# Optimization experiments

Hardware: AMD Instinct MI355X
Metric: run time of the kernel (lower is better)

The kernel has to match this reference:

```python
import jax, jax.numpy as jnp
import numpy as np

N, E, IN, HID, OUT, L = 50000, 800000, 128, 64, 40, 3


def setup_inputs() -> dict:
    key = jax.random.key(0)
    ks = jax.random.split(key, 10)
    x = jax.random.normal(ks[0], (N, IN), jnp.float32)
    edge_index = jax.random.randint(ks[1], (2, E), 0, N, dtype=jnp.int32)

    def u(k, shape, fan_in):
        s = 1.0 / np.sqrt(fan_in)
        return jax.random.uniform(k, shape, jnp.float32, -s, s)

    return {
        "x": x,
        "edge_index": edge_index,
        # former1 (NWGformerF): in -> hidden projection
        "Wf": u(ks[2], (IN, HID), IN),
        "bf": jnp.zeros((HID,), jnp.float32),
        # stacked GCNConv weights (hidden->hidden)
        "conv_W": u(ks[3], (L, HID, HID), HID),
        "conv_b": jnp.zeros((L, HID), jnp.float32),
        # residual linears
        "lin_W": u(ks[4], (L, HID, HID), HID),
        "lin_b": u(ks[5], (L, HID), HID),
        # batchnorm (eval mode: affine with running stats)
        "gamma": jnp.ones((L, HID), jnp.float32),
        "beta": jnp.zeros((L, HID), jnp.float32),
        "run_mean": jnp.zeros((L, HID), jnp.float32),
        "run_var": jnp.ones((L, HID), jnp.float32),
        # output head
        "pred_W": u(ks[6], (HID, OUT), HID),
        "pred_b": jnp.zeros((OUT,), jnp.float32),
    }


def reference(x, edge_index, Wf, bf, conv_W, conv_b, lin_W, lin_b,
              gamma, beta, run_mean, run_var, pred_W, pred_b):
    n = x.shape[0]
    src, dst = edge_index[0], edge_index[1]
    eps = 1e-5

    # GCN symmetric normalization with self-loops: deg over dst (+1 self loop)
    deg = jax.ops.segment_sum(jnp.ones(src.shape[0], x.dtype), dst,
                              num_segments=n) + 1.0
    dinv = jax.lax.rsqrt(deg)                      # [N]
    edge_coef = dinv[src] * dinv[dst]              # [E]
    self_coef = (dinv * dinv)[:, None]             # [N,1]

    def gcn(h, W, b):
        hw = h @ W                                 # [N,HID]
        agg = jax.ops.segment_sum(hw[src] * edge_coef[:, None], dst,
                                  num_segments=n)
        return agg + hw * self_coef + b

    # former1: in -> hidden (dropout is identity in eval mode)
    h = x @ Wf + bf

    for i in range(L):
        h = gcn(h, conv_W[i], conv_b[i]) + h @ lin_W[i] + lin_b[i]  # res
        h = (h - run_mean[i]) * (gamma[i] * jax.lax.rsqrt(run_var[i] + eps)) + beta[i]
        h = jax.nn.relu(h)

    return h @ pred_W + pred_b
```

## Files before the change

kernel.cpp:

```cpp
#include <hip/hip_runtime.h>
#include <hip/hip_bf16.h>
#include <hip/hip_fp16.h>

#define IN_DIM 128
#define HID 64
#define OUT_DIM 40
#define SPAD 68

typedef __hip_bfloat16 bf16;
typedef unsigned short u16;

__device__ __forceinline__ float b2f(bf16 v) { return __bfloat162float(v); }
__device__ __forceinline__ float relu_f(float x) { return 0.5f * (x + fabsf(x)); }
__device__ __forceinline__ float ldv(const void* p, int i, int is32) {
    return is32 ? ((const float*)p)[i] : b2f(((const bf16*)p)[i]);
}

__global__ void MPNNs_60198261620971_kernel() {}

__global__ void canary_k(float* out, int m) {
    int i = blockIdx.x * blockDim.x + threadIdx.x;
    if (i < m) out[i] = 1234.0f;
}

__global__ void detect_k(const unsigned int* __restrict__ rv, int* __restrict__ flag) {
    if (threadIdx.x == 0 && blockIdx.x == 0)
        flag[0] = (rv[0] == 0x3F800000u) ? 1 : 0;
}


__global__ void zero1_k(int* a, int n) {
    int i = blockIdx.x * blockDim.x + threadIdx.x;
    if (i < n) a[i] = 0;
}

__global__ void count_k(const int* __restrict__ dst, int* __restrict__ counts,
                        int* __restrict__ rank, int e, int n) {
    int i = blockIdx.x * blockDim.x + threadIdx.x;
    if (i < e) {
        int d = dst[i];
        int r = ((unsigned)d < (unsigned)n) ? atomicAdd(&counts[d], 1) : 0;
        rank[i] = r;
    }
}

__global__ void scan1_k(const int* __restrict__ counts, int* __restrict__ row_ptr,
                        int* __restrict__ psum, float* __restrict__ dinv, int n) {
    __shared__ int sdata[1024];
    int i = blockIdx.x * 1024 + threadIdx.x;
    int v = (i < n) ? counts[i] : 0;
    if (i < n) dinv[i] = rsqrtf((float)v + 1.0f);
    sdata[threadIdx.x] = v;
    __syncthreads();
    for (int off = 1; off < 1024; off <<= 1) {
        int t = (threadIdx.x >= off) ? sdata[threadIdx.x - off] : 0;
        __syncthreads();
        sdata[threadIdx.x] += t;
        __syncthreads();
    }
    if (i < n) row_ptr[i] = sdata[threadIdx.x] - v;
    if (threadIdx.x == 1023) psum[blockIdx.x] = sdata[1023];
}

__global__ void scan2_k(int* __restrict__ psum, int* __restrict__ row_ptr, int nb, int n) {
    __shared__ int sdata[1024];
    int v = (threadIdx.x < nb) ? psum[threadIdx.x] : 0;
    sdata[threadIdx.x] = v;
    __syncthreads();
    for (int off = 1; off < 1024; off <<= 1) {
        int t = (threadIdx.x >= off) ? sdata[threadIdx.x - off] : 0;
        __syncthreads();
        sdata[threadIdx.x] += t;
        __syncthreads();
    }
    if (threadIdx.x < nb) psum[threadIdx.x] = sdata[threadIdx.x] - v;
    if (threadIdx.x == 1023) row_ptr[n] = sdata[1023];
}

__global__ void scan3_k(int* __restrict__ row_ptr, const int* __restrict__ psum, int n) {
    int i = blockIdx.x * blockDim.x + threadIdx.x;
    if (i < n) row_ptr[i] += psum[i >> 10];
}

__global__ void fill_k(const int* __restrict__ src, const int* __restrict__ dst,
                       const int* __restrict__ row_ptr, const int* __restrict__ rank,
                       u16* __restrict__ col, int e, int n) {
    int i = blockIdx.x * blockDim.x + threadIdx.x;
    if (i < e) {
        int d = dst[i];
        if ((unsigned)d < (unsigned)n)
            col[row_ptr[d] + rank[i]] = (u16)src[i];
    }
}


__global__ __launch_bounds__(256) void former_k(const void* __restrict__ x,
                                                const void* __restrict__ Wf,
                                                const void* __restrict__ bfv,
                                                const int* __restrict__ dflag,
                                                float* __restrict__ h, int n) {
    __shared__ float sW[IN_DIM * HID];
    __shared__ float sx[64 * SPAD];
    int is32 = dflag[0];
    if (is32) {
        const float4* w4 = (const float4*)Wf;
        for (int i = threadIdx.x; i < IN_DIM * HID / 4; i += 256) ((float4*)sW)[i] = w4[i];
    } else {
        for (int i = threadIdx.x; i < IN_DIM * HID; i += 256) sW[i] = b2f(((const bf16*)Wf)[i]);
    }
    int tid = threadIdx.x, cg = tid & 15, rg = tid >> 4;
    int rowBase = blockIdx.x * 64;
    float acc[4][4];
    #pragma unroll
    for (int i = 0; i < 4; i++)
        #pragma unroll
        for (int j = 0; j < 4; j++) acc[i][j] = 0.f;

    for (int p = 0; p < 2; p++) {
        __syncthreads();
        #pragma unroll
        for (int pass = 0; pass < 4; pass++) {
            int r = pass * 16 + (tid >> 4);
            int c = (tid & 15) * 4;
            int gr = rowBase + r;
            float4 v = make_float4(0.f, 0.f, 0.f, 0.f);
            if (gr < n) {
                if (is32) v = *(const float4*)((const float*)x + (size_t)gr * IN_DIM + p * 64 + c);
                else {
                    const bf16* xb = (const bf16*)x + (size_t)gr * IN_DIM + p * 64 + c;
                    v = make_float4(b2f(xb[0]), b2f(xb[1]), b2f(xb[2]), b2f(xb[3]));
                }
            }
            *(float4*)&sx[r * SPAD + c] = v;
        }
        __syncthreads();
        for (int k = 0; k < 64; k += 4) {
            float4 hr[4], w[4];
            #pragma unroll
            for (int i = 0; i < 4; i++) hr[i] = *(float4*)&sx[(rg * 4 + i) * SPAD + k];
            #pragma unroll
            for (int j = 0; j < 4; j++) w[j] = *(float4*)&sW[(p * 64 + k + j) * HID + cg * 4];
            #pragma unroll
            for (int i = 0; i < 4; i++) {
                const float* hh = (const float*)&hr[i];
                #pragma unroll
                for (int j = 0; j < 4; j++) {
                    const float* ww = (const float*)&w[j];
                    acc[i][0] += hh[j] * ww[0];
                    acc[i][1] += hh[j] * ww[1];
                    acc[i][2] += hh[j] * ww[2];
                    acc[i][3] += hh[j] * ww[3];
                }
            }
        }
    }
    float b0 = ldv(bfv, cg * 4 + 0, is32), b1 = ldv(bfv, cg * 4 + 1, is32);
    float b2 = ldv(bfv, cg * 4 + 2, is32), b3 = ldv(bfv, cg * 4 + 3, is32);
    #pragma unroll
    for (int i = 0; i < 4; i++) {
        int r = rowBase + rg * 4 + i;
        if (r < n) {
            float4 o = make_float4(acc[i][0] + b0, acc[i][1] + b1, acc[i][2] + b2, acc[i][3] + b3);
            *(float4*)&h[(size_t)r * HID + cg * 4] = o;
        }
    }
}

__global__ __launch_bounds__(256) void dense_k(float* __restrict__ h,
                                               const void* __restrict__ convW,
                                               const void* __restrict__ linW,
                                               const void* __restrict__ convB,
                                               const void* __restrict__ linB,
                                               const int* __restrict__ dflag,
                                               const float* __restrict__ dinv,
                                               __half* __restrict__ hws, int n, int l) {
    __shared__ float sW1[HID * HID];
    __shared__ float sW2[HID * HID];
    __shared__ float sh[64 * SPAD];
    int is32 = dflag[0];
    int wOff = l * HID * HID, vOff = l * HID;
    if (is32) {
        const float4* a4 = (const float4*)((const float*)convW + wOff);
        const float4* b4 = (const float4*)((const float*)linW + wOff);
        for (int i = threadIdx.x; i < HID * HID / 4; i += 256) {
            ((float4*)sW1)[i] = a4[i];
            ((float4*)sW2)[i] = b4[i];
        }
    } else {
        for (int i = threadIdx.x; i < HID * HID; i += 256) {
            sW1[i] = b2f(((const bf16*)convW)[wOff + i]);
            sW2[i] = b2f(((const bf16*)linW)[wOff + i]);
        }
    }
    int tid = threadIdx.x, cg = tid & 15, rg = tid >> 4;
    int rowBase = blockIdx.x * 64;
    #pragma unroll
    for (int pass = 0; pass < 4; pass++) {
        int r = pass * 16 + (tid >> 4);
        int c = (tid & 15) * 4;
        int gr = rowBase + r;
        float4 v = (gr < n) ? *(const float4*)&h[(size_t)gr * HID + c] : make_float4(0.f, 0.f, 0.f, 0.f);
        *(float4*)&sh[r * SPAD + c] = v;
    }
    __syncthreads();
    float acc1[4][4], acc2[4][4];
    #pragma unroll
    for (int i = 0; i < 4; i++)
        #pragma unroll
        for (int j = 0; j < 4; j++) { acc1[i][j] = 0.f; acc2[i][j] = 0.f; }
    for (int k = 0; k < 64; k += 4) {
        float4 hr[4], w1[4], w2[4];
        #pragma unroll
        for (int i = 0; i < 4; i++) hr[i] = *(float4*)&sh[(rg * 4 + i) * SPAD + k];
        #pragma unroll
        for (int j = 0; j < 4; j++) {
            w1[j] = *(float4*)&sW1[(k + j) * HID + cg * 4];
            w2[j] = *(float4*)&sW2[(k + j) * HID + cg * 4];
        }
        #pragma unroll
        for (int i = 0; i < 4; i++) {
            const float* hh = (const float*)&hr[i];
            #pragma unroll
            for (int j = 0; j < 4; j++) {
                const float* p1 = (const float*)&w1[j];
                const float* p2 = (const float*)&w2[j];
                acc1[i][0] += hh[j] * p1[0]; acc1[i][1] += hh[j] * p1[1];
                acc1[i][2] += hh[j] * p1[2]; acc1[i][3] += hh[j] * p1[3];
                acc2[i][0] += hh[j] * p2[0]; acc2[i][1] += hh[j] * p2[1];
                acc2[i][2] += hh[j] * p2[2]; acc2[i][3] += hh[j] * p2[3];
            }
        }
    }
    float cb0 = ldv(convB, vOff + cg * 4 + 0, is32) + ldv(linB, vOff + cg * 4 + 0, is32);
    float cb1 = ldv(convB, vOff + cg * 4 + 1, is32) + ldv(linB, vOff + cg * 4 + 1, is32);
    float cb2 = ldv(convB, vOff + cg * 4 + 2, is32) + ldv(linB, vOff + cg * 4 + 2, is32);
    float cb3 = ldv(convB, vOff + cg * 4 + 3, is32) + ldv(linB, vOff + cg * 4 + 3, is32);
    #pragma unroll
    for (int i = 0; i < 4; i++) {
        int r = rowBase + rg * 4 + i;
        if (r < n) {
            float dv = dinv[r];
            __half2* hw2 = (__half2*)&hws[(size_t)r * HID + cg * 4];
            hw2[0] = __floats2half2_rn(acc1[i][0] * dv, acc1[i][1] * dv);
            hw2[1] = __floats2half2_rn(acc1[i][2] * dv, acc1[i][3] * dv);
            float4 o2 = make_float4(acc2[i][0] + cb0, acc2[i][1] + cb1, acc2[i][2] + cb2, acc2[i][3] + cb3);
            *(float4*)&h[(size_t)r * HID + cg * 4] = o2;
        }
    }
}

__global__ __launch_bounds__(256) void agg_k(const __half* __restrict__ hws,
                                             const float* __restrict__ dinv,
                                             const int* __restrict__ row_ptr,
                                             const u16* __restrict__ col,
                                             const void* __restrict__ gamma,
                                             const void* __restrict__ beta,
                                             const void* __restrict__ mean,
                                             const void* __restrict__ var,
                                             const int* __restrict__ dflag,
                                             float* __restrict__ h, int n, int l) {
    int gwave = (blockIdx.x * blockDim.x + threadIdx.x) >> 6;
    int lane = threadIdx.x & 63;
    int nw = (gridDim.x * blockDim.x) >> 6;
    int is32 = dflag[0];
    int vOff = l * HID;
    float mn = ldv(mean, vOff + lane, is32);
    float sc = ldv(gamma, vOff + lane, is32) * rsqrtf(ldv(var, vOff + lane, is32) + 1e-5f);
    float bt = ldv(beta, vOff + lane, is32);
    for (int v = gwave; v < n; v += nw) {
        int s0 = row_ptr[v], s1 = row_ptr[v + 1];
        float a0 = __half2float(hws[(size_t)v * HID + lane]);
        float a1 = 0.f, a2 = 0.f, a3 = 0.f, a4 = 0.f, a5 = 0.f, a6 = 0.f, a7 = 0.f;
        for (int j0 = s0; j0 < s1; j0 += 64) {
            int myidx = (j0 + lane < s1) ? (int)col[j0 + lane] : 0;
            int cnt = min(64, s1 - j0);
            int t = 0;
            for (; t + 8 <= cnt; t += 8) {
                int i0 = __shfl(myidx, t);
                int i1 = __shfl(myidx, t + 1);
                int i2 = __shfl(myidx, t + 2);
                int i3 = __shfl(myidx, t + 3);
                int i4 = __shfl(myidx, t + 4);
                int i5 = __shfl(myidx, t + 5);
                int i6 = __shfl(myidx, t + 6);
                int i7 = __shfl(myidx, t + 7);
                i0 = ((unsigned)i0 < (unsigned)n) ? i0 : 0;
                i1 = ((unsigned)i1 < (unsigned)n) ? i1 : 0;
                i2 = ((unsigned)i2 < (unsigned)n) ? i2 : 0;
                i3 = ((unsigned)i3 < (unsigned)n) ? i3 : 0;
                i4 = ((unsigned)i4 < (unsigned)n) ? i4 : 0;
                i5 = ((unsigned)i5 < (unsigned)n) ? i5 : 0;
                i6 = ((unsigned)i6 < (unsigned)n) ? i6 : 0;
                i7 = ((unsigned)i7 < (unsigned)n) ? i7 : 0;
                __half g0 = hws[(size_t)i0 * HID + lane];
                __half g1 = hws[(size_t)i1 * HID + lane];
                __half g2 = hws[(size_t)i2 * HID + lane];
                __half g3 = hws[(size_t)i3 * HID + lane];
                __half g4 = hws[(size_t)i4 * HID + lane];
                __half g5 = hws[(size_t)i5 * HID + lane];
                __half g6 = hws[(size_t)i6 * HID + lane];
                __half g7 = hws[(size_t)i7 * HID + lane];
                a0 += __half2float(g0); a1 += __half2float(g1);
                a2 += __half2float(g2); a3 += __half2float(g3);
                a4 += __half2float(g4); a5 += __half2float(g5);
                a6 += __half2float(g6); a7 += __half2float(g7);
            }
            for (; t < cnt; t++) {
                int s = __shfl(myidx, t);
                s = ((unsigned)s < (unsigned)n) ? s : 0;
                a0 += __half2float(hws[(size_t)s * HID + lane]);
            }
        }
        float acc = ((a0 + a1) + (a2 + a3)) + ((a4 + a5) + (a6 + a7));
        float val = dinv[v] * acc + h[(size_t)v * HID + lane];
        val = (val - mn) * sc + bt;
        h[(size_t)v * HID + lane] = relu_f(val);
    }
}

__global__ __launch_bounds__(256) void pred_k(const float* __restrict__ h,
                                              const void* __restrict__ pW,
                                              const void* __restrict__ pb,
                                              const int* __restrict__ dflag,
                                              void* __restrict__ out, int n) {
    __shared__ float sW[HID * OUT_DIM];
    __shared__ float sh[64 * SPAD];
    int is32 = dflag[0];
    if (is32) {
        const float4* w4 = (const float4*)pW;
        for (int i = threadIdx.x; i < HID * OUT_DIM / 4; i += 256) ((float4*)sW)[i] = w4[i];
    } else {
        for (int i = threadIdx.x; i < HID * OUT_DIM; i += 256) sW[i] = b2f(((const bf16*)pW)[i]);
    }
    int tid = threadIdx.x, cg = tid & 15, rg = tid >> 4;
    int rowBase = blockIdx.x * 64;
    #pragma unroll
    for (int pass = 0; pass < 4; pass++) {
        int r = pass * 16 + (tid >> 4);
        int c = (tid & 15) * 4;
        int gr = rowBase + r;
        float4 v = (gr < n) ? *(const float4*)&h[(size_t)gr * HID + c] : make_float4(0.f, 0.f, 0.f, 0.f);
        *(float4*)&sh[r * SPAD + c] = v;
    }
    __syncthreads();
    if (cg < 10) {
        float acc[4][4];
        #pragma unroll
        for (int i = 0; i < 4; i++)
            #pragma unroll
            for (int j = 0; j < 4; j++) acc[i][j] = 0.f;
        for (int k = 0; k < 64; k += 4) {
            float4 hr[4], w[4];
            #pragma unroll
            for (int i = 0; i < 4; i++) hr[i] = *(float4*)&sh[(rg * 4 + i) * SPAD + k];
            #pragma unroll
            for (int j = 0; j < 4; j++) w[j] = *(float4*)&sW[(k + j) * OUT_DIM + cg * 4];
            #pragma unroll
            for (int i = 0; i < 4; i++) {
                const float* hh = (const float*)&hr[i];
                #pragma unroll
                for (int j = 0; j < 4; j++) {
                    const float* ww = (const float*)&w[j];
                    acc[i][0] += hh[j] * ww[0];
                    acc[i][1] += hh[j] * ww[1];
                    acc[i][2] += hh[j] * ww[2];
                    acc[i][3] += hh[j] * ww[3];
                }
            }
        }
        float b0 = ldv(pb, cg * 4 + 0, is32), b1 = ldv(pb, cg * 4 + 1, is32);
        float b2 = ldv(pb, cg * 4 + 2, is32), b3 = ldv(pb, cg * 4 + 3, is32);
        #pragma unroll
        for (int i = 0; i < 4; i++) {
            int r = rowBase + rg * 4 + i;
            if (r < n) {
                if (is32) {
                    float4 o = make_float4(acc[i][0] + b0, acc[i][1] + b1, acc[i][2] + b2, acc[i][3] + b3);
                    *(float4*)((float*)out + (size_t)r * OUT_DIM + cg * 4) = o;
                } else {
                    bf16* ob = (bf16*)out + (size_t)r * OUT_DIM + cg * 4;
                    ob[0] = __float2bfloat16(acc[i][0] + b0);
                    ob[1] = __float2bfloat16(acc[i][1] + b1);
                    ob[2] = __float2bfloat16(acc[i][2] + b2);
                    ob[3] = __float2bfloat16(acc[i][3] + b3);
                }
            }
        }
    }
}


extern "C" void kernel_launch(void* const* d_in, const int* in_sizes, int n_in,
                              void* d_out, int out_size, void* d_ws, size_t ws_size,
                              hipStream_t stream) {
    const void* x     = d_in[0];
    const int*  ei    = (const int*)d_in[1];
    const void* Wf    = d_in[2];
    const void* bfv   = d_in[3];
    const void* convW = d_in[4];
    const void* convB = d_in[5];
    const void* linW  = d_in[6];
    const void* linB  = d_in[7];
    const void* gamma = d_in[8];
    const void* beta  = d_in[9];
    const void* rmean = d_in[10];
    const void* rvar  = d_in[11];
    const void* pW    = d_in[12];
    const void* pb    = d_in[13];

    const int n = in_sizes[0] / IN_DIM;
    const int e = in_sizes[1] / 2;
    const int L = in_sizes[5] / HID;

    const int* src = ei;
    const int* dst = ei + e;

    char* ws = (char*)d_ws;
    size_t off = 0;
    auto take = [&](size_t bytes) {
        char* p = ws + off;
        off = (off + bytes + 255) & ~(size_t)255;
        return p;
    };
    float*  h       = (float*)take((size_t)n * HID * 4);
    __half* hws     = (__half*)take((size_t)n * HID * 2);
    float*  dinv    = (float*)take((size_t)n * 4);
    int*    counts  = (int*)take((size_t)n * 4);
    int*    row_ptr = (int*)take((size_t)(n + 1) * 4);
    int*    rank    = (int*)take((size_t)e * 4);
    u16*    colbuf  = (u16*)take((size_t)e * 2);
    int*    psum    = (int*)take(1024 * 4);
    int*    dflag   = (int*)take(256);

    if (off > ws_size || n > 65535) {
        canary_k<<<(out_size + 255) / 256, 256, 0, stream>>>((float*)d_out, out_size);
        return;
    }

    const int eblocks = (e + 255) / 256;
    const int nblocks = (n + 255) / 256;
    const int nb1024  = (n + 1023) / 1024;
    const int nb64    = (n + 63) / 64;

    detect_k<<<1, 64, 0, stream>>>((const unsigned int*)rvar, dflag);

    zero1_k<<<nblocks, 256, 0, stream>>>(counts, n);
    count_k<<<eblocks, 256, 0, stream>>>(dst, counts, rank, e, n);
    scan1_k<<<nb1024, 1024, 0, stream>>>(counts, row_ptr, psum, dinv, n);
    scan2_k<<<1, 1024, 0, stream>>>(psum, row_ptr, nb1024, n);
    scan3_k<<<nblocks, 256, 0, stream>>>(row_ptr, psum, n);
    fill_k<<<eblocks, 256, 0, stream>>>(src, dst, row_ptr, rank, colbuf, e, n);

    former_k<<<nb64, 256, 0, stream>>>(x, Wf, bfv, dflag, h, n);

    for (int l = 0; l < L; l++) {
        dense_k<<<nb64, 256, 0, stream>>>(h, convW, linW, convB, linB,
                                          dflag, dinv, hws, n, l);
        agg_k<<<2048, 256, 0, stream>>>(hws, dinv, row_ptr, colbuf,
                                        gamma, beta, rmean, rvar, dflag, h, n, l);
    }

    pred_k<<<nb64, 256, 0, stream>>>(h, pW, pb, dflag, (void*)d_out, n);
}
```

Measured before the change: 328.5 us.

## Use MFMA f16 for dense layer, pack degree counts to 16-bit, fuse zero/detect

Replaces the FP32 scalar-FMA dense kernel with MFMA 16x16x32 f16 instructions, keeping transposed f16 weights in shared memory and converting h to f16 on load. Degree counting now uses packed 16-bit counters with two nodes per 32-bit atomic, and ranks are stored as u16, which halves that traffic. The zero-init and dtype-detect kernels are merged into one launch. The f16 inputs lower matmul precision, the new epilogue writes scalar elements instead of vector stores, and the 16-bit counters assume in-degree below 65536.

```diff
diff --git a/kernel.cpp b/kernel.cpp
--- a/kernel.cpp
+++ b/kernel.cpp
@@ -9,6 +9,9 @@
 
 typedef __hip_bfloat16 bf16;
 typedef unsigned short u16;
+typedef _Float16 f16;
+typedef __attribute__((ext_vector_type(8))) _Float16 f16x8;
+typedef __attribute__((ext_vector_type(4))) float f32x4;
 
 __device__ __forceinline__ float b2f(bf16 v) { return __bfloat162float(v); }
 __device__ __forceinline__ float relu_f(float x) { return 0.5f * (x + fabsf(x)); }
@@ -23,32 +26,35 @@
     if (i < m) out[i] = 1234.0f;
 }
 
-__global__ void detect_k(const unsigned int* __restrict__ rv, int* __restrict__ flag) {
-    if (threadIdx.x == 0 && blockIdx.x == 0)
-        flag[0] = (rv[0] == 0x3F800000u) ? 1 : 0;
-}
-
-
-__global__ void zero1_k(int* a, int n) {
+
+__global__ void zerodetect_k(unsigned int* __restrict__ c2, int n2,
+                             const unsigned int* __restrict__ rv, int* __restrict__ flag) {
     int i = blockIdx.x * blockDim.x + threadIdx.x;
-    if (i < n) a[i] = 0;
-}
-
-__global__ void count_k(const int* __restrict__ dst, int* __restrict__ counts,
-                        int* __restrict__ rank, int e, int n) {
+    if (i < n2) c2[i] = 0;
+    if (i == 0) flag[0] = (rv[0] == 0x3F800000u) ? 1 : 0;
+}
+
+__global__ void count_k(const int* __restrict__ dst, unsigned int* __restrict__ c2,
+                        u16* __restrict__ rank, int e, int n) {
     int i = blockIdx.x * blockDim.x + threadIdx.x;
     if (i < e) {
         int d = dst[i];
-        int r = ((unsigned)d < (unsigned)n) ? atomicAdd(&counts[d], 1) : 0;
+        u16 r = 0;
+        if ((unsigned)d < (unsigned)n) {
+            int sh = (d & 1) * 16;
+            unsigned old = atomicAdd(&c2[d >> 1], 1u << sh);
+            r = (u16)((old >> sh) & 0xFFFFu);
+        }
         rank[i] = r;
     }
 }
 
-__global__ void scan1_k(const int* __restrict__ counts, int* __restrict__ row_ptr,
+__global__ void scan1_k(const unsigned int* __restrict__ c2, int* __restrict__ row_ptr,
                         int* __restrict__ psum, float* __restrict__ dinv, int n) {
     __shared__ int sdata[1024];
     int i = blockIdx.x * 1024 + threadIdx.x;
-    int v = (i < n) ? counts[i] : 0;
+    int v = 0;
+    if (i < n) v = (int)((c2[i >> 1] >> ((i & 1) * 16)) & 0xFFFFu);
     if (i < n) dinv[i] = rsqrtf((float)v + 1.0f);
     sdata[threadIdx.x] = v;
     __syncthreads();
@@ -83,13 +89,13 @@
 }
 
 __global__ void fill_k(const int* __restrict__ src, const int* __restrict__ dst,
-                       const int* __restrict__ row_ptr, const int* __restrict__ rank,
+                       const int* __restrict__ row_ptr, const u16* __restrict__ rank,
                        u16* __restrict__ col, int e, int n) {
     int i = blockIdx.x * blockDim.x + threadIdx.x;
     if (i < e) {
         int d = dst[i];
         if ((unsigned)d < (unsigned)n)
-            col[row_ptr[d] + rank[i]] = (u16)src[i];
+            col[row_ptr[d] + (int)rank[i]] = (u16)src[i];
     }
 }
 
@@ -174,77 +180,61 @@
                                                const int* __restrict__ dflag,
                                                const float* __restrict__ dinv,
                                                __half* __restrict__ hws, int n, int l) {
-    __shared__ float sW1[HID * HID];
-    __shared__ float sW2[HID * HID];
-    __shared__ float sh[64 * SPAD];
+    __shared__ __align__(16) f16 wT[2][HID][72];
     int is32 = dflag[0];
     int wOff = l * HID * HID, vOff = l * HID;
-    if (is32) {
-        const float4* a4 = (const float4*)((const float*)convW + wOff);
-        const float4* b4 = (const float4*)((const float*)linW + wOff);
-        for (int i = threadIdx.x; i < HID * HID / 4; i += 256) {
-            ((float4*)sW1)[i] = a4[i];
-            ((float4*)sW2)[i] = b4[i];
-        }
-    } else {
-        for (int i = threadIdx.x; i < HID * HID; i += 256) {
-            sW1[i] = b2f(((const bf16*)convW)[wOff + i]);
-            sW2[i] = b2f(((const bf16*)linW)[wOff + i]);
-        }
-    }
-    int tid = threadIdx.x, cg = tid & 15, rg = tid >> 4;
-    int rowBase = blockIdx.x * 64;
-    #pragma unroll
-    for (int pass = 0; pass < 4; pass++) {
-        int r = pass * 16 + (tid >> 4);
-        int c = (tid & 15) * 4;
-        int gr = rowBase + r;
-        float4 v = (gr < n) ? *(const float4*)&h[(size_t)gr * HID + c] : make_float4(0.f, 0.f, 0.f, 0.f);
-        *(float4*)&sh[r * SPAD + c] = v;
+    for (int i = threadIdx.x; i < HID * HID; i += 256) {
+        int k = i >> 6, nn = i & 63;
+        wT[0][nn][k] = (f16)ldv(convW, wOff + i, is32);
+        wT[1][nn][k] = (f16)ldv(linW, wOff + i, is32);
     }
     __syncthreads();
-    float acc1[4][4], acc2[4][4];
-    #pragma unroll
-    for (int i = 0; i < 4; i++)
+    int wave = threadIdx.x >> 6, lane = threadIdx.x & 63;
+    int m = lane & 15, quad = lane >> 4;
+    int row0 = blockIdx.x * 64 + wave * 16;
+    if (row0 >= n) return;
+    int ar = row0 + m;
+    const float* hp = h + (size_t)((ar < n) ? ar : 0) * HID;
+    float4 v0 = *(const float4*)(hp + quad * 8);
+    float4 v1 = *(const float4*)(hp + quad * 8 + 4);
+    float4 v2 = *(const float4*)(hp + 32 + quad * 8);
+    float4 v3 = *(const float4*)(hp + 32 + quad * 8 + 4);
+    f16x8 a0 = { (f16)v0.x, (f16)v0.y, (f16)v0.z, (f16)v0.w,
+                 (f16)v1.x, (f16)v1.y, (f16)v1.z, (f16)v1.w };
+    f16x8 a1 = { (f16)v2.x, (f16)v2.y, (f16)v2.z, (f16)v2.w,
+                 (f16)v3.x, (f16)v3.y, (f16)v3.z, (f16)v3.w };
+    f32x4 acc[2][4];
+    #pragma unroll
+    for (int t = 0; t < 2; t++)
         #pragma unroll
-        for (int j = 0; j < 4; j++) { acc1[i][j] = 0.f; acc2[i][j] = 0.f; }
-    for (int k = 0; k < 64; k += 4) {
-        float4 hr[4], w1[4], w2[4];
-        #pragma unroll
-        for (int i = 0; i < 4; i++) hr[i] = *(float4*)&sh[(rg * 4 + i) * SPAD + k];
-        #pragma unroll
-        for (int j = 0; j < 4; j++) {
-            w1[j] = *(float4*)&sW1[(k + j) * HID + cg * 4];
-            w2[j] = *(float4*)&sW2[(k + j) * HID + cg * 4];
-        }
-        #pragma unroll
-        for (int i = 0; i < 4; i++) {
-            const float* hh = (const float*)&hr[i];
-            #pragma unroll
-            for (int j = 0; j < 4; j++) {
-                const float* p1 = (const float*)&w1[j];
-                const float* p2 = (const float*)&w2[j];
-                acc1[i][0] += hh[j] * p1[0]; acc1[i][1] += hh[j] * p1[1];
-                acc1[i][2] += hh[j] * p1[2]; acc1[i][3] += hh[j] * p1[3];
-                acc2[i][0] += hh[j] * p2[0]; acc2[i][1] += hh[j] * p2[1];
-                acc2[i][2] += hh[j] * p2[2]; acc2[i][3] += hh[j] * p2[3];
-            }
-        }
-    }
-    float cb0 = ldv(convB, vOff + cg * 4 + 0, is32) + ldv(linB, vOff + cg * 4 + 0, is32);
-    float cb1 = ldv(convB, vOff + cg * 4 + 1, is32) + ldv(linB, vOff + cg * 4 + 1, is32);
-    float cb2 = ldv(convB, vOff + cg * 4 + 2, is32) + ldv(linB, vOff + cg * 4 + 2, is32);
-    float cb3 = ldv(convB, vOff + cg * 4 + 3, is32) + ldv(linB, vOff + cg * 4 + 3, is32);
-    #pragma unroll
-    for (int i = 0; i < 4; i++) {
-        int r = rowBase + rg * 4 + i;
-        if (r < n) {
-            float dv = dinv[r];
-            __half2* hw2 = (__half2*)&hws[(size_t)r * HID + cg * 4];
-            hw2[0] = __floats2half2_rn(acc1[i][0] * dv, acc1[i][1] * dv);
-            hw2[1] = __floats2half2_rn(acc1[i][2] * dv, acc1[i][3] * dv);
-            float4 o2 = make_float4(acc2[i][0] + cb0, acc2[i][1] + cb1, acc2[i][2] + cb2, acc2[i][3] + cb3);
-            *(float4*)&h[(size_t)r * HID + cg * 4] = o2;
+        for (int ct = 0; ct < 4; ct++) acc[t][ct] = (f32x4){0.f, 0.f, 0.f, 0.f};
+    #pragma unroll
+    for (int ct = 0; ct < 4; ct++) {
+        int nn = ct * 16 + m;
+        f16x8 b00 = *(const f16x8*)&wT[0][nn][quad * 8];
+        f16x8 b01 = *(const f16x8*)&wT[0][nn][32 + quad * 8];
+        f16x8 b10 = *(const f16x8*)&wT[1][nn][quad * 8];
+        f16x8 b11 = *(const f16x8*)&wT[1][nn][32 + quad * 8];
+        acc[0][ct] = __builtin_amdgcn_mfma_f32_16x16x32_f16(a0, b00, acc[0][ct], 0, 0, 0);
+        acc[0][ct] = __builtin_amdgcn_mfma_f32_16x16x32_f16(a1, b01, acc[0][ct], 0, 0, 0);
+        acc[1][ct] = __builtin_amdgcn_mfma_f32_16x16x32_f16(a0, b10, acc[1][ct], 0, 0, 0);
+        acc[1][ct] = __builtin_amdgcn_mfma_f32_16x16x32_f16(a1, b11, acc[1][ct], 0, 0, 0);
+    }
+    float cbv[4];
+    #pragma unroll
+    for (int ct = 0; ct < 4; ct++)
+        cbv[ct] = ldv(convB, vOff + ct * 16 + m, is32) + ldv(linB, vOff + ct * 16 + m, is32);
+    #pragma unroll
+    for (int r = 0; r < 4; r++) {
+        int row = row0 + quad * 4 + r;
+        if (row < n) {
+            float dv = dinv[row];
+            #pragma unroll
+            for (int ct = 0; ct < 4; ct++) {
+                int colx = ct * 16 + m;
+                hws[(size_t)row * HID + colx] = __float2half(acc[0][ct][r] * dv);
+                h[(size_t)row * HID + colx] = acc[1][ct][r] + cbv[ct];
+            }
         }
     }
 }
@@ -411,6 +401,7 @@
     const int n = in_sizes[0] / IN_DIM;
     const int e = in_sizes[1] / 2;
     const int L = in_sizes[5] / HID;
+    const int n2 = (n + 1) / 2;
 
     const int* src = ei;
     const int* dst = ei + e;
@@ -422,15 +413,15 @@
         off = (off + bytes + 255) & ~(size_t)255;
         return p;
     };
-    float*  h       = (float*)take((size_t)n * HID * 4);
-    __half* hws     = (__half*)take((size_t)n * HID * 2);
-    float*  dinv    = (float*)take((size_t)n * 4);
-    int*    counts  = (int*)take((size_t)n * 4);
-    int*    row_ptr = (int*)take((size_t)(n + 1) * 4);
-    int*    rank    = (int*)take((size_t)e * 4);
-    u16*    colbuf  = (u16*)take((size_t)e * 2);
-    int*    psum    = (int*)take(1024 * 4);
-    int*    dflag   = (int*)take(256);
+    float*        h       = (float*)take((size_t)n * HID * 4);
+    __half*       hws     = (__half*)take((size_t)n * HID * 2);
+    float*        dinv    = (float*)take((size_t)n * 4);
+    unsigned int* c2      = (unsigned int*)take((size_t)n2 * 4);
+    int*          row_ptr = (int*)take((size_t)(n + 1) * 4);
+    u16*          rank    = (u16*)take((size_t)e * 2);
+    u16*          colbuf  = (u16*)take((size_t)e * 2);
+    int*          psum    = (int*)take(1024 * 4);
+    int*          dflag   = (int*)take(256);
 
     if (off > ws_size || n > 65535) {
         canary_k<<<(out_size + 255) / 256, 256, 0, stream>>>((float*)d_out, out_size);
@@ -442,11 +433,9 @@
     const int nb1024  = (n + 1023) / 1024;
     const int nb64    = (n + 63) / 64;
 
-    detect_k<<<1, 64, 0, stream>>>((const unsigned int*)rvar, dflag);
-
-    zero1_k<<<nblocks, 256, 0, stream>>>(counts, n);
-    count_k<<<eblocks, 256, 0, stream>>>(dst, counts, rank, e, n);
-    scan1_k<<<nb1024, 1024, 0, stream>>>(counts, row_ptr, psum, dinv, n);
+    zerodetect_k<<<(n2 + 255) / 256, 256, 0, stream>>>(c2, n2, (const unsigned int*)rvar, dflag);
+    count_k<<<eblocks, 256, 0, stream>>>(dst, c2, rank, e, n);
+    scan1_k<<<nb1024, 1024, 0, stream>>>(c2, row_ptr, psum, dinv, n);
     scan2_k<<<1, 1024, 0, stream>>>(psum, row_ptr, nb1024, n);
     scan3_k<<<nblocks, 256, 0, stream>>>(row_ptr, psum, n);
     fill_k<<<eblocks, 256, 0, stream>>>(src, dst, row_ptr, rank, colbuf, e, n);
```

Result: no change. 328.0 us (-0.1%).
